# Kernel tuning notes

Hardware: AMD Instinct MI355X
Metric: run time of the kernel (lower is better)

The kernel has to match this reference:

```python
import jax, jax.numpy as jnp
import numpy as np

B, S, E, H = 16, 256, 4096, 16
D = E // H  # 256; module's matmul pattern requires S == D and B == H


def setup_inputs() -> dict:
    rng = jax.random.key(0)
    k0, k1, k2, k3, k4 = jax.random.split(rng, 5)
    return {
        "query": jax.random.normal(k0, (B, S, E), jnp.float32),
        "key": jax.random.normal(k1, (B, S, E), jnp.float32),
        "value": jax.random.normal(k2, (B, S, E), jnp.float32),
        # out_proj: torch nn.Linear(E, E) -> y = x @ W.T + b
        "out_w": jax.random.normal(k3, (E, E), jnp.float32) * 0.02,
        "out_b": jnp.zeros((E,), jnp.float32),
    }


def reference(query, key, value, out_w, out_b):
    scale = D ** -0.5
    # split heads: [B, S, E] -> [B, H, S, D]
    q = (query * scale).reshape(B, S, H, D).transpose(0, 2, 1, 3)
    k = key.reshape(B, S, H, D).transpose(0, 2, 1, 3)
    v = value.reshape(B, S, H, D).transpose(0, 2, 1, 3)
    # torch.matmul(q_head, k_head) with NO transpose: contracts q's D with k's S
    # (valid because S == D). aw: [B, H, S, D]
    aw = jnp.einsum('bhit,bhtj->bhij', q, k)
    # attn_weights.transpose(0, 1): [B, H, ...] -> [H, B, ...]
    aw = jnp.swapaxes(aw, 0, 1)
    # eval mode path: softmax over last dim (no dropout)
    aw = jax.nn.softmax(aw, axis=-1)
    # torch.matmul(aw [H,B,S,D], v [B,H,S,D]): batch dims broadcast because B == H,
    # pairing elementwise -> out[x,y] = aw[x,y] @ v[x,y]
    out = jnp.einsum('xyit,xytj->xyij', aw, v)
    # transpose(1, 2) then reshape to (B, S, E)
    out = jnp.swapaxes(out, 1, 2).reshape(B, S, E)
    # out_proj
    return out @ out_w.T + out_b
```

## Files before the change

### kernel.cpp

```cpp
#include <hip/hip_runtime.h>

#define AS1 __attribute__((address_space(1)))
#define AS3 __attribute__((address_space(3)))

typedef __bf16 bf16x8 __attribute__((ext_vector_type(8)));
typedef float f32x4 __attribute__((ext_vector_type(4)));

__device__ __forceinline__ unsigned short f2bf(float f) {
  unsigned int u = __builtin_bit_cast(unsigned int, f);
  u += 0x7fffu + ((u >> 16) & 1u);
  return (unsigned short)(u >> 16);
}

__global__ __launch_bounds__(256) void kv_transpose(
    const float* __restrict__ key, const float* __restrict__ value,
    unsigned short* __restrict__ KT2, unsigned short* __restrict__ VT2) {
  __shared__ float tr[32 * 33];
  const int tid = threadIdx.x;
  const int ts  = blockIdx.y;
  const int pp  = blockIdx.x >> 3;
  const int s   = blockIdx.x & 7;
  const int b   = ts ? (pp >> 4) : (pp & 15);
  const int h   = ts ? (pp & 15) : (pp >> 4);
  const float* src = (ts ? value : key) + ((size_t)(b * 256 + s * 32)) * 4096 + h * 256;
  unsigned short* dst = (ts ? VT2 : KT2) + (size_t)(pp * 8 + s) * 8192;
  const int tt = tid >> 3;
  const int q8 = tid & 7;
  for (int jb = 0; jb < 8; ++jb) {
    float4 v = *(const float4*)(src + (size_t)tt * 4096 + jb * 32 + q8 * 4);
    tr[tt * 33 + q8 * 4 + 0] = v.x;
    tr[tt * 33 + q8 * 4 + 1] = v.y;
    tr[tt * 33 + q8 * 4 + 2] = v.z;
    tr[tt * 33 + q8 * 4 + 3] = v.w;
    __syncthreads();
    ushort4 o;
    o.x = f2bf(tr[(q8 * 4 + 0) * 33 + tt]);
    o.y = f2bf(tr[(q8 * 4 + 1) * 33 + tt]);
    o.z = f2bf(tr[(q8 * 4 + 2) * 33 + tt]);
    o.w = f2bf(tr[(q8 * 4 + 3) * 33 + tt]);
    *(ushort4*)(dst + (jb * 32 + tt) * 32 + q8 * 4) = o;
    __syncthreads();
  }
}

__global__ __launch_bounds__(256, 2) void attn_kernel(
    const float* __restrict__ qin, const unsigned short* __restrict__ KT2,
    const unsigned short* __restrict__ VT2, unsigned short* __restrict__ attn) {
  __shared__ __align__(16) unsigned short kv[8192];
  __shared__ __align__(16) unsigned short plds[4 * 16 * 264];

  const int tid  = threadIdx.x;
  const int lane = tid & 63;
  const int wave = tid >> 6;
  const int li   = lane & 15;
  const int ks   = lane >> 4;

  const int bid = blockIdx.x;
  const int pp  = (bid & 7) * 32 + ((bid >> 3) & 31);
  const int ib  = bid >> 8;
  const int x = pp >> 4, y = pp & 15;
  const int i0 = ib * 64 + wave * 16;

  bf16x8 qf[8];
  {
    const float* qrow = qin + ((size_t)(y * 256 + i0 + li)) * 4096 + x * 256 + ks * 8;
#pragma unroll
    for (int s = 0; s < 8; ++s) {
      float4 v0 = *(const float4*)(qrow + s * 32);
      float4 v1 = *(const float4*)(qrow + s * 32 + 4);
      union { bf16x8 v; unsigned short u[8]; } t;
      t.u[0] = f2bf(v0.x * 0.0625f); t.u[1] = f2bf(v0.y * 0.0625f);
      t.u[2] = f2bf(v0.z * 0.0625f); t.u[3] = f2bf(v0.w * 0.0625f);
      t.u[4] = f2bf(v1.x * 0.0625f); t.u[5] = f2bf(v1.y * 0.0625f);
      t.u[6] = f2bf(v1.z * 0.0625f); t.u[7] = f2bf(v1.w * 0.0625f);
      qf[s] = t.v;
    }
  }

  const f32x4 vzero = {0.f, 0.f, 0.f, 0.f};
  f32x4 sacc[16];
#pragma unroll
  for (int f = 0; f < 16; ++f) sacc[f] = vzero;

  const unsigned short* ktile = KT2 + (size_t)pp * 65536;
#pragma unroll
  for (int s = 0; s < 8; ++s) {
    __syncthreads();
#pragma unroll
    for (int cc = 0; cc < 4; ++cc) {
      const unsigned short* g = ktile + (size_t)s * 8192 + (cc * 256 + tid) * 8;
      __builtin_amdgcn_global_load_lds((AS1 unsigned int*)g,
          (AS3 unsigned int*)((AS3 char*)kv + cc * 4096 + wave * 1024), 16, 0, 0);
    }
    __syncthreads();
#pragma unroll
    for (int f = 0; f < 16; ++f) {
      bf16x8 bfr = *(const bf16x8*)&kv[(f * 16 + li) * 32 + ks * 8];
      sacc[f] = __builtin_amdgcn_mfma_f32_16x16x32_bf16(qf[s], bfr, sacc[f], 0, 0, 0);
    }
  }

  float sm[4];
#pragma unroll
  for (int qi = 0; qi < 4; ++qi) {
    float m = sacc[0][qi];
#pragma unroll
    for (int f = 1; f < 16; ++f) m = fmaxf(m, sacc[f][qi]);
    m = fmaxf(m, __shfl_xor(m, 1));
    m = fmaxf(m, __shfl_xor(m, 2));
    m = fmaxf(m, __shfl_xor(m, 4));
    m = fmaxf(m, __shfl_xor(m, 8));
    float ssum = 0.f;
#pragma unroll
    for (int f = 0; f < 16; ++f) {
      float pv = __expf(sacc[f][qi] - m);
      sacc[f][qi] = pv;
      ssum += pv;
    }
    ssum += __shfl_xor(ssum, 1);
    ssum += __shfl_xor(ssum, 2);
    ssum += __shfl_xor(ssum, 4);
    ssum += __shfl_xor(ssum, 8);
    sm[qi] = ssum;
  }

  unsigned short* pw = plds + wave * 4224;
#pragma unroll
  for (int f = 0; f < 16; ++f)
#pragma unroll
    for (int qi = 0; qi < 4; ++qi)
      pw[(ks * 4 + qi) * 264 + f * 16 + li] = f2bf(sacc[f][qi]);

  f32x4 oacc[16];
#pragma unroll
  for (int f = 0; f < 16; ++f) oacc[f] = vzero;
  const unsigned short* vtile = VT2 + (size_t)pp * 65536;
  const unsigned short* pr = plds + wave * 4224 + li * 264;
#pragma unroll
  for (int s2 = 0; s2 < 8; ++s2) {
    __syncthreads();
#pragma unroll
    for (int cc = 0; cc < 4; ++cc) {
      const unsigned short* g = vtile + (size_t)s2 * 8192 + (cc * 256 + tid) * 8;
      __builtin_amdgcn_global_load_lds((AS1 unsigned int*)g,
          (AS3 unsigned int*)((AS3 char*)kv + cc * 4096 + wave * 1024), 16, 0, 0);
    }
    __syncthreads();
    bf16x8 afr = *(const bf16x8*)&pr[s2 * 32 + ks * 8];
#pragma unroll
    for (int f = 0; f < 16; ++f) {
      bf16x8 bfr = *(const bf16x8*)&kv[(f * 16 + li) * 32 + ks * 8];
      oacc[f] = __builtin_amdgcn_mfma_f32_16x16x32_bf16(afr, bfr, oacc[f], 0, 0, 0);
    }
  }

  float rs4[4];
#pragma unroll
  for (int qi = 0; qi < 4; ++qi) rs4[qi] = 1.0f / sm[qi];
  unsigned short* abase = attn + (size_t)(x * 256 + i0 + ks * 4) * 4096 + y * 256 + li;
#pragma unroll
  for (int f = 0; f < 16; ++f)
#pragma unroll
    for (int qi = 0; qi < 4; ++qi)
      abase[(size_t)qi * 4096 + f * 16] = f2bf(oacc[f][qi] * rs4[qi]);
}

__global__ __launch_bounds__(256) void convw(const float* __restrict__ w,
                                             unsigned short* __restrict__ o) {
  const int i = blockIdx.x * 256 + threadIdx.x;
  const float4* s = (const float4*)w + (size_t)i * 2;
  float4 v0 = s[0], v1 = s[1];
  uint4 pk;
  pk.x = (unsigned)f2bf(v0.x) | ((unsigned)f2bf(v0.y) << 16);
  pk.y = (unsigned)f2bf(v0.z) | ((unsigned)f2bf(v0.w) << 16);
  pk.z = (unsigned)f2bf(v1.x) | ((unsigned)f2bf(v1.y) << 16);
  pk.w = (unsigned)f2bf(v1.z) | ((unsigned)f2bf(v1.w) << 16);
  *((uint4*)o + i) = pk;
}

__global__ __launch_bounds__(512, 2) void proj_gemm8(
    const unsigned short* __restrict__ A, const unsigned short* __restrict__ W,
    const float* __restrict__ bias, float* __restrict__ out) {
  __shared__ __align__(1024) char lds[131072];

  const int tid  = threadIdx.x;
  const int lane = tid & 63;
  const int w    = tid >> 6;
  const int li   = lane & 15;
  const int ks   = lane >> 4;
  const int wr   = w >> 2;
  const int wc   = w & 3;
  const int LB   = (li * 64 + ks * 16) ^ (((li >> 3) & 1) << 5);

  const int bid = blockIdx.x;
  const int swz = (bid & 7) * 32 + (bid >> 3);
  const int m0b = (swz >> 4) * 256, n0b = (swz & 15) * 256;

  unsigned sA[2][2], sB[2][2];
#pragma unroll
  for (int i2 = 0; i2 < 2; ++i2) {
    int P = w * 2048 + i2 * 1024 + lane * 16;
    int L = P ^ (((P >> 9) & 1) << 5);
    int kk = L >> 13, row = (L >> 6) & 127, cb = L & 63;
#pragma unroll
    for (int h = 0; h < 2; ++h) {
      sA[h][i2] = (unsigned)((m0b + h * 128 + row) * 8192 + kk * 64 + cb);
      sB[h][i2] = (unsigned)((n0b + h * 128 + row) * 8192 + kk * 64 + cb);
    }
  }
  const char* Ac = (const char*)A;
  const char* Wc = (const char*)W;
  AS3 char* L3 = (AS3 char*)lds;

  const f32x4 vzero = {0.f, 0.f, 0.f, 0.f};
  f32x4 acc[8][4];
#pragma unroll
  for (int m = 0; m < 8; ++m)
#pragma unroll
    for (int n = 0; n < 4; ++n) acc[m][n] = vzero;

#define STAGE_A(h, i2, koffb, bufo) \
  __builtin_amdgcn_global_load_lds((AS1 unsigned int*)(Ac + sA[h][i2] + (koffb)), \
      (AS3 unsigned int*)(L3 + (bufo) + (h) * 16384 + w * 2048 + (i2) * 1024), 16, 0, 0)
#define STAGE_B(h, i2, koffb, bufo) \
  __builtin_amdgcn_global_load_lds((AS1 unsigned int*)(Wc + sB[h][i2] + (koffb)), \
      (AS3 unsigned int*)(L3 + 65536 + (bufo) + (h) * 16384 + w * 2048 + (i2) * 1024), 16, 0, 0)
#define RD_A(m, kk) (*(const bf16x8*)(lds + aoff + wr * 16384 + (kk) * 8192 + (m) * 1024 + LB))
#define RD_B(n, kk) (*(const bf16x8*)(lds + boff + (wc >> 1) * 16384 + (kk) * 8192 + \
                                      (wc & 1) * 4096 + (n) * 1024 + LB))
#define MFMA(a, b, c) __builtin_amdgcn_mfma_f32_16x16x32_bf16((a), (b), (c), 0, 0, 0)

#pragma unroll
  for (int tt = 0; tt < 2; ++tt) {
#pragma unroll
    for (int h = 0; h < 2; ++h)
#pragma unroll
      for (int i2 = 0; i2 < 2; ++i2) {
        STAGE_A(h, i2, tt * 128u, tt * 32768);
        STAGE_B(h, i2, tt * 128u, tt * 32768);
      }
  }
  asm volatile("s_waitcnt vmcnt(8)" ::: "memory");
  __builtin_amdgcn_s_barrier();

  bf16x8 afr[4][2], bA[2][2], bB[2][2];

  for (int t = 0; t < 64; ++t) {
    const int cur  = t & 1;
    const int aoff = cur * 32768;
    const int boff = 65536 + cur * 32768;
    const int ts   = (t + 2 < 64) ? t + 2 : 63;
    const unsigned koff = (unsigned)ts * 128u;

#pragma unroll
    for (int m = 0; m < 4; ++m)
#pragma unroll
      for (int kk = 0; kk < 2; ++kk) afr[m][kk] = RD_A(m, kk);
#pragma unroll
    for (int n = 0; n < 2; ++n)
#pragma unroll
      for (int kk = 0; kk < 2; ++kk) bA[n][kk] = RD_B(n, kk);
    __builtin_amdgcn_s_setprio(1);
#pragma unroll
    for (int m = 0; m < 4; ++m)
#pragma unroll
      for (int n = 0; n < 2; ++n)
#pragma unroll
        for (int kk = 0; kk < 2; ++kk)
          acc[m][n] = MFMA(afr[m][kk], bA[n][kk], acc[m][n]);
    __builtin_amdgcn_s_setprio(0);

#pragma unroll
    for (int n = 0; n < 2; ++n)
#pragma unroll
      for (int kk = 0; kk < 2; ++kk) bB[n][kk] = RD_B(n + 2, kk);
    __builtin_amdgcn_s_setprio(1);
#pragma unroll
    for (int m = 0; m < 4; ++m)
#pragma unroll
      for (int n = 0; n < 2; ++n)
#pragma unroll
        for (int kk = 0; kk < 2; ++kk)
          acc[m][n + 2] = MFMA(afr[m][kk], bB[n][kk], acc[m][n + 2]);
    __builtin_amdgcn_s_setprio(0);

#pragma unroll
    for (int m = 0; m < 4; ++m)
#pragma unroll
      for (int kk = 0; kk < 2; ++kk) afr[m][kk] = RD_A(m + 4, kk);
    __builtin_amdgcn_s_setprio(1);
#pragma unroll
    for (int m = 0; m < 4; ++m)
#pragma unroll
      for (int n = 0; n < 2; ++n)
#pragma unroll
        for (int kk = 0; kk < 2; ++kk)
          acc[m + 4][n + 2] = MFMA(afr[m][kk], bB[n][kk], acc[m + 4][n + 2]);
    __builtin_amdgcn_s_setprio(0);

    asm volatile("s_waitcnt lgkmcnt(0)" ::: "memory");
    __builtin_amdgcn_s_barrier();
#pragma unroll
    for (int h = 0; h < 2; ++h)
#pragma unroll
      for (int i2 = 0; i2 < 2; ++i2) {
        STAGE_B(h, i2, koff, aoff);
        STAGE_A(h, i2, koff, aoff);
      }

    __builtin_amdgcn_s_setprio(1);
#pragma unroll
    for (int m = 0; m < 4; ++m)
#pragma unroll
      for (int n = 0; n < 2; ++n)
#pragma unroll
        for (int kk = 0; kk < 2; ++kk)
          acc[m + 4][n] = MFMA(afr[m][kk], bA[n][kk], acc[m + 4][n]);
    __builtin_amdgcn_s_setprio(0);

    asm volatile("s_waitcnt vmcnt(8)" ::: "memory");
    __builtin_amdgcn_s_barrier();
  }

  float bv[4];
#pragma unroll
  for (int n = 0; n < 4; ++n) bv[n] = bias[n0b + wc * 64 + n * 16 + li];
#pragma unroll
  for (int m = 0; m < 8; ++m) {
#pragma unroll
    for (int qi = 0; qi < 4; ++qi) {
      const int row = m0b + wr * 128 + m * 16 + ks * 4 + qi;
      float* orow = out + (size_t)row * 4096 + n0b + wc * 64 + li;
#pragma unroll
      for (int n = 0; n < 4; ++n) orow[n * 16] = acc[m][n][qi] + bv[n];
    }
  }
#undef STAGE_A
#undef STAGE_B
#undef RD_A
#undef RD_B
#undef MFMA
}

extern "C" void kernel_launch(void* const* d_in, const int* in_sizes, int n_in,
                              void* d_out, int out_size, void* d_ws, size_t ws_size,
                              hipStream_t stream) {
  const float* q = (const float*)d_in[0];
  const float* k = (const float*)d_in[1];
  const float* v = (const float*)d_in[2];
  const float* w = (const float*)d_in[3];
  const float* b = (const float*)d_in[4];
  float* out = (float*)d_out;
  char* ws = (char*)d_ws;

  unsigned short* attn = (unsigned short*)ws;
  unsigned short* KT2  = (unsigned short*)(ws + (size_t)33554432);
  unsigned short* VT2  = (unsigned short*)(ws + (size_t)67108864);
  unsigned short* wbf  = KT2;

  kv_transpose<<<dim3(2048, 2), 256, 0, stream>>>(k, v, KT2, VT2);
  attn_kernel<<<1024, 256, 0, stream>>>(q, KT2, VT2, attn);
  convw<<<8192, 256, 0, stream>>>(w, wbf);
  proj_gemm8<<<256, 512, 0, stream>>>(attn, wbf, b, out);
}
```

Before: 246.8 us.

## Restructure projection GEMM LDS layout and interleave staggered global-to-LDS staging

Rewrites the output-projection GEMM's shared-memory tile layout so each row holds a full 128-byte K slice with a new XOR swizzle. Global-to-LDS loads are split into quarter-tile chunks issued between the MFMA phases, with A staged one step ahead and B two steps ahead, instead of one bulk staging point per iteration. The intent is to hide load latency inside the compute and spread memory traffic evenly. The cost is extra barriers per iteration, which may add synchronisation stalls.

```diff
diff --git a/kernel.cpp b/kernel.cpp
--- a/kernel.cpp
+++ b/kernel.cpp
@@ -190,22 +190,25 @@
   const int ks   = lane >> 4;
   const int wr   = w >> 2;
   const int wc   = w & 3;
-  const int LB   = (li * 64 + ks * 16) ^ (((li >> 3) & 1) << 5);
+  const int liLB = li * 128 + ((ks * 16) ^ (((li >> 2) & 1) << 5));
+  const int bB   = 32768 + (wc >> 1) * 16384 + (wc & 1) * 8192;
 
   const int bid = blockIdx.x;
   const int swz = (bid & 7) * 32 + (bid >> 3);
   const int m0b = (swz >> 4) * 256, n0b = (swz & 15) * 256;
 
-  unsigned sA[2][2], sB[2][2];
-#pragma unroll
-  for (int i2 = 0; i2 < 2; ++i2) {
-    int P = w * 2048 + i2 * 1024 + lane * 16;
+  unsigned srcA[2][2], srcB[2][2];
+  int dstP[2];
+#pragma unroll
+  for (int j = 0; j < 2; ++j) {
+    int P = j * 8192 + tid * 16;
     int L = P ^ (((P >> 9) & 1) << 5);
-    int kk = L >> 13, row = (L >> 6) & 127, cb = L & 63;
+    int row = L >> 7, col = L & 127;
+    dstP[j] = P;
 #pragma unroll
     for (int h = 0; h < 2; ++h) {
-      sA[h][i2] = (unsigned)((m0b + h * 128 + row) * 8192 + kk * 64 + cb);
-      sB[h][i2] = (unsigned)((n0b + h * 128 + row) * 8192 + kk * 64 + cb);
+      srcA[h][j] = (unsigned)((m0b + h * 128 + row) * 8192 + col);
+      srcB[h][j] = (unsigned)((n0b + h * 128 + row) * 8192 + col);
     }
   }
   const char* Ac = (const char*)A;
@@ -219,47 +222,52 @@
 #pragma unroll
     for (int n = 0; n < 4; ++n) acc[m][n] = vzero;
 
-#define STAGE_A(h, i2, koffb, bufo) \
-  __builtin_amdgcn_global_load_lds((AS1 unsigned int*)(Ac + sA[h][i2] + (koffb)), \
-      (AS3 unsigned int*)(L3 + (bufo) + (h) * 16384 + w * 2048 + (i2) * 1024), 16, 0, 0)
-#define STAGE_B(h, i2, koffb, bufo) \
-  __builtin_amdgcn_global_load_lds((AS1 unsigned int*)(Wc + sB[h][i2] + (koffb)), \
-      (AS3 unsigned int*)(L3 + 65536 + (bufo) + (h) * 16384 + w * 2048 + (i2) * 1024), 16, 0, 0)
-#define RD_A(m, kk) (*(const bf16x8*)(lds + aoff + wr * 16384 + (kk) * 8192 + (m) * 1024 + LB))
-#define RD_B(n, kk) (*(const bf16x8*)(lds + boff + (wc >> 1) * 16384 + (kk) * 8192 + \
-                                      (wc & 1) * 4096 + (n) * 1024 + LB))
+#define STG_A(h, kt, bufo) do {                                                \
+    _Pragma("unroll") for (int j = 0; j < 2; ++j)                              \
+      __builtin_amdgcn_global_load_lds(                                        \
+          (AS1 unsigned int*)(Ac + srcA[h][j] + (unsigned)(kt) * 128u),        \
+          (AS3 unsigned int*)(L3 + (bufo) + (h) * 16384 + dstP[j]), 16, 0, 0); \
+  } while (0)
+#define STG_B(h, kt, bufo) do {                                                \
+    _Pragma("unroll") for (int j = 0; j < 2; ++j)                              \
+      __builtin_amdgcn_global_load_lds(                                        \
+          (AS1 unsigned int*)(Wc + srcB[h][j] + (unsigned)(kt) * 128u),        \
+          (AS3 unsigned int*)(L3 + (bufo) + 32768 + (h) * 16384 + dstP[j]),    \
+          16, 0, 0);                                                           \
+  } while (0)
+#define RD_A(bufo, m, kk) \
+  (*(const bf16x8*)(lds + (bufo) + wr * 16384 + (m) * 2048 + (kk) * 64 + liLB))
+#define RD_B(bufo, n, kk) \
+  (*(const bf16x8*)(lds + (bufo) + bB + (n) * 2048 + (kk) * 64 + liLB))
 #define MFMA(a, b, c) __builtin_amdgcn_mfma_f32_16x16x32_bf16((a), (b), (c), 0, 0, 0)
-
-#pragma unroll
-  for (int tt = 0; tt < 2; ++tt) {
-#pragma unroll
-    for (int h = 0; h < 2; ++h)
-#pragma unroll
-      for (int i2 = 0; i2 < 2; ++i2) {
-        STAGE_A(h, i2, tt * 128u, tt * 32768);
-        STAGE_B(h, i2, tt * 128u, tt * 32768);
-      }
-  }
-  asm volatile("s_waitcnt vmcnt(8)" ::: "memory");
-  __builtin_amdgcn_s_barrier();
-
-  bf16x8 afr[4][2], bA[2][2], bB[2][2];
+#define BAR() __builtin_amdgcn_s_barrier()
+#define LGKM0() asm volatile("s_waitcnt lgkmcnt(0)" ::: "memory")
+
+  STG_A(0, 0, 0); STG_A(1, 0, 0); STG_B(0, 0, 0); STG_B(1, 0, 0);
+  STG_B(0, 1, 65536); STG_B(1, 1, 65536);
+  asm volatile("s_waitcnt vmcnt(4)" ::: "memory");
+  BAR();
+
+  bf16x8 Af[4][2], B0[2][2], B1[2][2];
 
   for (int t = 0; t < 64; ++t) {
-    const int cur  = t & 1;
-    const int aoff = cur * 32768;
-    const int boff = 65536 + cur * 32768;
-    const int ts   = (t + 2 < 64) ? t + 2 : 63;
-    const unsigned koff = (unsigned)ts * 128u;
-
-#pragma unroll
-    for (int m = 0; m < 4; ++m)
-#pragma unroll
-      for (int kk = 0; kk < 2; ++kk) afr[m][kk] = RD_A(m, kk);
+    const int p = (t & 1) * 65536;
+    const int q = 65536 - p;
+    const int k1 = (t < 63) ? t + 1 : 63;
+    const int k2 = (t < 62) ? t + 2 : 63;
+
+#pragma unroll
+    for (int m = 0; m < 4; ++m)
+#pragma unroll
+      for (int kk = 0; kk < 2; ++kk) Af[m][kk] = RD_A(p, m, kk);
 #pragma unroll
     for (int n = 0; n < 2; ++n)
 #pragma unroll
-      for (int kk = 0; kk < 2; ++kk) bA[n][kk] = RD_B(n, kk);
+      for (int kk = 0; kk < 2; ++kk) B0[n][kk] = RD_B(p, n, kk);
+    STG_A(0, k1, q);
+    asm volatile("s_waitcnt lgkmcnt(8)" ::: "memory");
+    BAR();
+    LGKM0();
     __builtin_amdgcn_s_setprio(1);
 #pragma unroll
     for (int m = 0; m < 4; ++m)
@@ -267,13 +275,17 @@
       for (int n = 0; n < 2; ++n)
 #pragma unroll
         for (int kk = 0; kk < 2; ++kk)
-          acc[m][n] = MFMA(afr[m][kk], bA[n][kk], acc[m][n]);
+          acc[m][n] = MFMA(Af[m][kk], B0[n][kk], acc[m][n]);
     __builtin_amdgcn_s_setprio(0);
+    BAR();
 
 #pragma unroll
     for (int n = 0; n < 2; ++n)
 #pragma unroll
-      for (int kk = 0; kk < 2; ++kk) bB[n][kk] = RD_B(n + 2, kk);
+      for (int kk = 0; kk < 2; ++kk) B1[n][kk] = RD_B(p, n + 2, kk);
+    STG_A(1, k1, q);
+    BAR();
+    LGKM0();
     __builtin_amdgcn_s_setprio(1);
 #pragma unroll
     for (int m = 0; m < 4; ++m)
@@ -281,13 +293,17 @@
       for (int n = 0; n < 2; ++n)
 #pragma unroll
         for (int kk = 0; kk < 2; ++kk)
-          acc[m][n + 2] = MFMA(afr[m][kk], bB[n][kk], acc[m][n + 2]);
+          acc[m][n + 2] = MFMA(Af[m][kk], B1[n][kk], acc[m][n + 2]);
     __builtin_amdgcn_s_setprio(0);
-
-#pragma unroll
-    for (int m = 0; m < 4; ++m)
-#pragma unroll
-      for (int kk = 0; kk < 2; ++kk) afr[m][kk] = RD_A(m + 4, kk);
+    BAR();
+
+#pragma unroll
+    for (int m = 0; m < 4; ++m)
+#pragma unroll
+      for (int kk = 0; kk < 2; ++kk) Af[m][kk] = RD_A(p, m + 4, kk);
+    STG_B(0, k2, p);
+    BAR();
+    LGKM0();
     __builtin_amdgcn_s_setprio(1);
 #pragma unroll
     for (int m = 0; m < 4; ++m)
@@ -295,19 +311,12 @@
       for (int n = 0; n < 2; ++n)
 #pragma unroll
         for (int kk = 0; kk < 2; ++kk)
-          acc[m + 4][n + 2] = MFMA(afr[m][kk], bB[n][kk], acc[m + 4][n + 2]);
+          acc[m + 4][n + 2] = MFMA(Af[m][kk], B1[n][kk], acc[m + 4][n + 2]);
     __builtin_amdgcn_s_setprio(0);
-
-    asm volatile("s_waitcnt lgkmcnt(0)" ::: "memory");
-    __builtin_amdgcn_s_barrier();
-#pragma unroll
-    for (int h = 0; h < 2; ++h)
-#pragma unroll
-      for (int i2 = 0; i2 < 2; ++i2) {
-        STAGE_B(h, i2, koff, aoff);
-        STAGE_A(h, i2, koff, aoff);
-      }
-
+    BAR();
+
+    STG_B(1, k2, p);
+    BAR();
     __builtin_amdgcn_s_setprio(1);
 #pragma unroll
     for (int m = 0; m < 4; ++m)
@@ -315,11 +324,10 @@
       for (int n = 0; n < 2; ++n)
 #pragma unroll
         for (int kk = 0; kk < 2; ++kk)
-          acc[m + 4][n] = MFMA(afr[m][kk], bA[n][kk], acc[m + 4][n]);
+          acc[m + 4][n] = MFMA(Af[m][kk], B0[n][kk], acc[m + 4][n]);
     __builtin_amdgcn_s_setprio(0);
-
-    asm volatile("s_waitcnt vmcnt(8)" ::: "memory");
-    __builtin_amdgcn_s_barrier();
+    asm volatile("s_waitcnt vmcnt(4)" ::: "memory");
+    BAR();
   }
 
   float bv[4];
@@ -335,11 +343,13 @@
       for (int n = 0; n < 4; ++n) orow[n * 16] = acc[m][n][qi] + bv[n];
     }
   }
-#undef STAGE_A
-#undef STAGE_B
+#undef STG_A
+#undef STG_B
 #undef RD_A
 #undef RD_B
 #undef MFMA
+#undef BAR
+#undef LGKM0
 }
 
 extern "C" void kernel_launch(void* const* d_in, const int* in_sizes, int n_in,
```

Measured after the change: 241.1 us. 1.02x faster.
